# Kernel optimization log

Hardware: AMD Instinct MI355X
Metric: run time of the kernel (lower is better)

The kernel has to match this reference:

```python
import jax, jax.numpy as jnp
import numpy as np

N_VERT = 163842  # icosphere level-7 vertex count
IN_FEATS = 64
OUT_FEATS = 64
BATCH = 2
K = 7  # center vertex + 6 one-ring neighbors


def setup_inputs() -> dict:
    key = jax.random.key(0)
    k1, k2, k3, k4 = jax.random.split(key, 4)
    x = jax.random.normal(k1, (N_VERT, IN_FEATS, BATCH), dtype=jnp.float32)
    neigh_orders = jax.random.randint(k2, (K * N_VERT,), 0, N_VERT, dtype=jnp.int64)
    W = jax.random.normal(k3, (OUT_FEATS, K * IN_FEATS), dtype=jnp.float32) * 0.05
    b = jax.random.normal(k4, (OUT_FEATS,), dtype=jnp.float32) * 0.05
    return {"x": x, "neigh_orders": neigh_orders, "W": W, "b": b}


def reference(x, neigh_orders, W, b):
    # x: [N, C, B]; neigh_orders: [7N] flat indices, grouped per-vertex (n*7 + k)
    N = x.shape[0]
    C = x.shape[1]
    idx = neigh_orders.reshape(N, K)            # [N, 7]
    gathered = x[idx]                           # [N, 7, C, B] irregular gather
    Wr = W.reshape(W.shape[0], K, C)            # [O, 7, C] matches flatten order (k*C + c)
    # out[n, o, b] = sum_{k,c} gathered[n,k,c,b] * W[o, k*C + c] + b[o]
    out = jnp.einsum("nkcb,okc->nob", gathered, Wr) + b[None, :, None]
    return out  # [N, O, B]
```

## Files before the change

kernel.cpp:

```cpp
#include <hip/hip_runtime.h>

#define NV      163842
#define CIN     64
#define KN      7
#define KDIM    448
#define KSTEPS  14
#define VPC     16
#define ROWS    32
#define ASTRIDE 456

typedef short  short8 __attribute__((ext_vector_type(8)));
typedef float  f32x4  __attribute__((ext_vector_type(4)));

static __device__ __forceinline__ unsigned int pack_bf16(float a, float b) {
#if __has_builtin(__builtin_amdgcn_cvt_pk_bf16_f32)
    typedef __bf16 bf16x2 __attribute__((ext_vector_type(2)));
    union { bf16x2 v; unsigned int u; } cv;
    cv.v = __builtin_amdgcn_cvt_pk_bf16_f32(a, b);
    return cv.u;
#else
    unsigned int ua = __float_as_uint(a);
    unsigned int ub = __float_as_uint(b);
    ua = (ua + 0x7FFFu + ((ua >> 16) & 1u)) >> 16;
    ub = (ub + 0x7FFFu + ((ub >> 16) & 1u)) & 0xFFFF0000u;
    return ua | ub;
#endif
}

__global__ __launch_bounds__(256)
void xcast(const float* __restrict__ x, unsigned int* __restrict__ xt, int nf4)
{
    const int f = blockIdx.x * 256 + threadIdx.x;
    if (f >= nf4) return;
    const float4 g = ((const float4*)x)[f];
    const int v = f >> 5;
    const int r = f & 31;
    xt[v * 32 + r]           = pack_bf16(g.x, g.z);
    xt[NV * 32 + v * 32 + r] = pack_bf16(g.y, g.w);
}

__global__ __launch_bounds__(256, 4)
void onering_mfma_bf16(const unsigned short* __restrict__ xt,
                       const int* __restrict__ neigh,
                       const float* __restrict__ W,
                       const float* __restrict__ bias,
                       float* __restrict__ out,
                       int nchunks)
{
    __shared__ unsigned short A_lds[ROWS * ASTRIDE];
    __shared__ float          C_lds[VPC * 128];

    const int tid  = threadIdx.x;
    const int lane = tid & 63;
    const int w    = tid >> 6;
    const int ncol = lane & 15;
    const int kgrp = lane >> 4;

    short8 bfrag[KSTEPS];
    {
        const int o = w * 16 + ncol;
#pragma unroll
        for (int s = 0; s < KSTEPS; ++s) {
            const int kb = s * 32 + kgrp * 8;
            const float4* wp = (const float4*)(W + o * KDIM + kb);
            float4 w0 = wp[0];
            float4 w1 = wp[1];
            union { short8 v; unsigned int u[4]; } pk;
            pk.u[0] = pack_bf16(w0.x, w0.y);
            pk.u[1] = pack_bf16(w0.z, w0.w);
            pk.u[2] = pack_bf16(w1.x, w1.y);
            pk.u[3] = pack_bf16(w1.z, w1.w);
            bfrag[s] = pk.v;
        }
    }
    const float biasv = bias[w * 16 + ncol];

    const int l8 = tid & 7;
    int nidx[7];
    int lbyte[7];
    int soff[7];
#pragma unroll
    for (int i = 0; i < 7; ++i) {
        const int seg = (tid >> 3) + 32 * i;
        const int row = seg / 7;
        const int k   = seg - row * 7;
        const int lv  = row >> 1, bb = row & 1;
        nidx[i]  = lv * KN + k;
        lbyte[i] = row * (ASTRIDE * 2) + k * 128 + l8 * 16;
        soff[i]  = bb * (NV * 64) + l8 * 8;
    }

    for (int ch = blockIdx.x; ch < nchunks; ch += gridDim.x) {
        const int vb  = ch * VPC;
        const int vb7 = vb * KN;

        __syncthreads();

#pragma unroll
        for (int i = 0; i < 7; ++i) {
            const int gi = vb7 + nidx[i];
            const int vi = (gi < NV * KN) ? neigh[gi] : 0;
            const short8 v = *(const short8*)(xt + soff[i] + vi * 64);
            *(short8*)((char*)A_lds + lbyte[i]) = v;
        }
        __syncthreads();

        f32x4 acc0 = {0.f, 0.f, 0.f, 0.f};
        f32x4 acc1 = {0.f, 0.f, 0.f, 0.f};
#pragma unroll
        for (int s = 0; s < KSTEPS; ++s) {
            const int kb = s * 32 + kgrp * 8;
            const short8 a0 = *(const short8*)&A_lds[ncol * ASTRIDE + kb];
            const short8 a1 = *(const short8*)&A_lds[(16 + ncol) * ASTRIDE + kb];
            acc0 = __builtin_amdgcn_mfma_f32_16x16x32_bf16(a0, bfrag[s], acc0, 0, 0, 0);
            acc1 = __builtin_amdgcn_mfma_f32_16x16x32_bf16(a1, bfrag[s], acc1, 0, 0, 0);
        }

        const int o2 = (w * 16 + ncol) * 2;
#pragma unroll
        for (int j = 0; j < 4; ++j) {
            const int r  = kgrp * 4 + j;
            C_lds[(r >> 1) * 128 + o2 + (r & 1)] = acc0[j] + biasv;
            const int r2 = 16 + r;
            C_lds[(r2 >> 1) * 128 + o2 + (r2 & 1)] = acc1[j] + biasv;
        }
        __syncthreads();

        float4* dst = (float4*)(out + vb * 128);
#pragma unroll
        for (int it = 0; it < 2; ++it) {
            const int fidx = tid + 256 * it;
            if (vb + (fidx >> 5) < NV)
                dst[fidx] = ((const float4*)C_lds)[fidx];
        }
    }
}

__global__ __launch_bounds__(256, 4)
void onering_mfma_f32(const float* __restrict__ x,
                      const int* __restrict__ neigh,
                      const float* __restrict__ W,
                      const float* __restrict__ bias,
                      float* __restrict__ out,
                      int nchunks)
{
    __shared__ unsigned short A_lds[ROWS * ASTRIDE];
    const int tid  = threadIdx.x;
    const int lane = tid & 63;
    const int w    = tid >> 6;
    const int ncol = lane & 15;
    const int kgrp = lane >> 4;

    short8 bfrag[KSTEPS];
    {
        const int o = w * 16 + ncol;
#pragma unroll
        for (int s = 0; s < KSTEPS; ++s) {
            const int kb = s * 32 + kgrp * 8;
            const float4* wp = (const float4*)(W + o * KDIM + kb);
            float4 w0 = wp[0];
            float4 w1 = wp[1];
            union { short8 v; unsigned int u[4]; } pk;
            pk.u[0] = pack_bf16(w0.x, w0.y);
            pk.u[1] = pack_bf16(w0.z, w0.w);
            pk.u[2] = pack_bf16(w1.x, w1.y);
            pk.u[3] = pack_bf16(w1.z, w1.w);
            bfrag[s] = pk.v;
        }
    }
    const float biasv = bias[w * 16 + ncol];
    const int off4  = tid & 31;
    const int sbase = tid >> 5;

    for (int ch = blockIdx.x; ch < nchunks; ch += gridDim.x) {
        const int vb = ch * VPC;
        __syncthreads();
#pragma unroll
        for (int i = 0; i < 14; ++i) {
            const int s  = sbase + 8 * i;
            const int lv = s / 7;
            const int k  = s - lv * 7;
            const int n  = vb + lv;
            int vi = 0;
            if (n < NV) vi = neigh[n * KN + k];
            const float4 g = ((const float4*)x)[vi * 32 + off4];
            const int base = k * 64 + 2 * off4;
            ((unsigned int*)A_lds)[((lv * 2)     * ASTRIDE + base) >> 1] = pack_bf16(g.x, g.z);
            ((unsigned int*)A_lds)[((lv * 2 + 1) * ASTRIDE + base) >> 1] = pack_bf16(g.y, g.w);
        }
        __syncthreads();
        f32x4 acc0 = {0.f, 0.f, 0.f, 0.f};
        f32x4 acc1 = {0.f, 0.f, 0.f, 0.f};
#pragma unroll
        for (int s = 0; s < KSTEPS; ++s) {
            const int kb = s * 32 + kgrp * 8;
            const short8 a0 = *(const short8*)&A_lds[ncol * ASTRIDE + kb];
            const short8 a1 = *(const short8*)&A_lds[(16 + ncol) * ASTRIDE + kb];
            acc0 = __builtin_amdgcn_mfma_f32_16x16x32_bf16(a0, bfrag[s], acc0, 0, 0, 0);
            acc1 = __builtin_amdgcn_mfma_f32_16x16x32_bf16(a1, bfrag[s], acc1, 0, 0, 0);
        }
        const int o = w * 16 + ncol;
#pragma unroll
        for (int j = 0; j < 4; ++j) {
            const int r = kgrp * 4 + j;
            {
                const int lv = r >> 1, bb = r & 1, n = vb + lv;
                if (n < NV) out[n * 128 + o * 2 + bb] = acc0[j] + biasv;
            }
            {
                const int m = 16 + r;
                const int lv = m >> 1, bb = m & 1, n = vb + lv;
                if (n < NV) out[n * 128 + o * 2 + bb] = acc1[j] + biasv;
            }
        }
    }
}

extern "C" void kernel_launch(void* const* d_in, const int* in_sizes, int n_in,
                              void* d_out, int out_size, void* d_ws, size_t ws_size,
                              hipStream_t stream) {
    const float* x     = (const float*)d_in[0];
    const int*   neigh = (const int*)d_in[1];
    const float* W     = (const float*)d_in[2];
    const float* bias  = (const float*)d_in[3];
    float*       out   = (float*)d_out;

    const int nchunks = (NV + VPC - 1) / VPC;
    const size_t need = (size_t)2 * NV * 64 * sizeof(unsigned short);

    if (ws_size >= need) {
        unsigned short* xt = (unsigned short*)d_ws;
        const int nf4 = NV * 32;
        xcast<<<dim3((nf4 + 255) / 256), dim3(256), 0, stream>>>(x, (unsigned int*)xt, nf4);
        onering_mfma_bf16<<<dim3(2560), dim3(256), 0, stream>>>(xt, neigh, W, bias, out, nchunks);
    } else {
        onering_mfma_f32<<<dim3(2560), dim3(256), 0, stream>>>(x, neigh, W, bias, out, nchunks);
    }
}
```

Measured before the change: 248.3 us.

## Software-pipeline gather with register prefetch of next chunk's indices and rows

```diff
diff --git a/kernel.cpp b/kernel.cpp
--- a/kernel.cpp
+++ b/kernel.cpp
@@ -3,6 +3,7 @@
 #define NV      163842
 #define CIN     64
 #define KN      7
+#define NKMAX   (NV * KN)
 #define KDIM    448
 #define KSTEPS  14
 #define VPC     16
@@ -27,6 +28,10 @@
 #endif
 }
 
+static __device__ __forceinline__ void bar_lgkm() {
+    asm volatile("s_waitcnt lgkmcnt(0)\n\ts_barrier" ::: "memory");
+}
+
 __global__ __launch_bounds__(256)
 void xcast(const float* __restrict__ x, unsigned int* __restrict__ xt, int nf4)
 {
@@ -39,7 +44,7 @@
     xt[NV * 32 + v * 32 + r] = pack_bf16(g.y, g.w);
 }
 
-__global__ __launch_bounds__(256, 4)
+__global__ __launch_bounds__(256, 3)
 void onering_mfma_bf16(const unsigned short* __restrict__ xt,
                        const int* __restrict__ neigh,
                        const float* __restrict__ W,
@@ -55,6 +60,7 @@
     const int w    = tid >> 6;
     const int ncol = lane & 15;
     const int kgrp = lane >> 4;
+    const int G    = gridDim.x;
 
     short8 bfrag[KSTEPS];
     {
@@ -90,20 +96,42 @@
         soff[i]  = bb * (NV * 64) + l8 * 8;
     }
 
-    for (int ch = blockIdx.x; ch < nchunks; ch += gridDim.x) {
-        const int vb  = ch * VPC;
-        const int vb7 = vb * KN;
-
-        __syncthreads();
-
+    const int ch0 = blockIdx.x;
+    int    I[7];
+    short8 R[7];
+
+#pragma unroll
+    for (int i = 0; i < 7; ++i) {
+        int gi = ch0 * (VPC * KN) + nidx[i];
+        I[i] = neigh[gi < NKMAX ? gi : 0];
+    }
+#pragma unroll
+    for (int i = 0; i < 7; ++i)
+        R[i] = *(const short8*)(xt + soff[i] + I[i] * 64);
+#pragma unroll
+    for (int i = 0; i < 7; ++i) {
+        int gi = (ch0 + G) * (VPC * KN) + nidx[i];
+        I[i] = neigh[gi < NKMAX ? gi : 0];
+    }
+
+    for (int ch = ch0; ch < nchunks; ch += G) {
+        const int vb = ch * VPC;
+
+        bar_lgkm();
+
+#pragma unroll
+        for (int i = 0; i < 7; ++i)
+            *(short8*)((char*)A_lds + lbyte[i]) = R[i];
+#pragma unroll
+        for (int i = 0; i < 7; ++i)
+            R[i] = *(const short8*)(xt + soff[i] + I[i] * 64);
 #pragma unroll
         for (int i = 0; i < 7; ++i) {
-            const int gi = vb7 + nidx[i];
-            const int vi = (gi < NV * KN) ? neigh[gi] : 0;
-            const short8 v = *(const short8*)(xt + soff[i] + vi * 64);
-            *(short8*)((char*)A_lds + lbyte[i]) = v;
-        }
-        __syncthreads();
+            int gi = (ch + 2 * G) * (VPC * KN) + nidx[i];
+            I[i] = neigh[gi < NKMAX ? gi : 0];
+        }
+
+        bar_lgkm();
 
         f32x4 acc0 = {0.f, 0.f, 0.f, 0.f};
         f32x4 acc1 = {0.f, 0.f, 0.f, 0.f};
@@ -124,7 +152,8 @@
             const int r2 = 16 + r;
             C_lds[(r2 >> 1) * 128 + o2 + (r2 & 1)] = acc1[j] + biasv;
         }
-        __syncthreads();
+
+        bar_lgkm();
 
         float4* dst = (float4*)(out + vb * 128);
 #pragma unroll
```

New measurement: 214.8 us. 13.5% less time.
